# Kernel tuning notes

Measured on AMD Instinct MI355X. Metric: run time of the kernel, lower is better.

The kernel has to match this reference:

```python
import jax, jax.numpy as jnp
import numpy as np

N, E, DIM, HEADS = 50000, 600000, 128, 4
C = DIM // HEADS  # per-head channels = 32
NEG_SLOPE = 0.2
LN_EPS = 1e-5


def setup_inputs() -> dict:
    key = jax.random.key(0)
    ks = jax.random.split(key, 6)
    x = jax.random.normal(ks[0], (N, DIM), dtype=jnp.float32)
    edge_index = jax.random.randint(ks[1], (2, E), 0, N, dtype=jnp.int32)
    W = jax.random.normal(ks[2], (DIM, DIM), dtype=jnp.float32) / np.sqrt(DIM).astype(np.float32)
    b = jnp.zeros((DIM,), jnp.float32)
    att_src = jax.random.normal(ks[3], (HEADS, C), dtype=jnp.float32) * 0.1
    att_dst = jax.random.normal(ks[4], (HEADS, C), dtype=jnp.float32) * 0.1
    gamma = jnp.ones((DIM,), jnp.float32)
    beta = jnp.zeros((DIM,), jnp.float32)
    return {"x": x, "W": W, "b": b, "att_src": att_src, "att_dst": att_dst,
            "gamma": gamma, "beta": beta, "edge_index": edge_index}


def _gat_conv(x, W, b, att_src, att_dst, src, dst):
    # linear projection, per-head view: [N, H, C]
    h = (x @ W).reshape(N, HEADS, C)
    # per-node attention logits: [N, H]
    a_s = jnp.einsum('nhc,hc->nh', h, att_src)
    a_d = jnp.einsum('nhc,hc->nh', h, att_dst)
    # per-edge logits with leaky relu: [Etot, H]
    e = jax.nn.leaky_relu(a_s[src] + a_d[dst], negative_slope=NEG_SLOPE)
    # segment softmax over incoming edges of each dst node
    m = jax.ops.segment_max(e, dst, num_segments=N)
    ez = jnp.exp(e - m[dst])
    denom = jax.ops.segment_sum(ez, dst, num_segments=N) + 1e-16
    alpha = ez / denom[dst]  # [Etot, H]
    # weighted scatter-aggregation: [N, H, C]
    out = jax.ops.segment_sum(alpha[:, :, None] * h[src], dst, num_segments=N)
    return out.reshape(N, DIM) + b


def reference(x, W, b, att_src, att_dst, gamma, beta, edge_index):
    # add self loops (PyG GATConv default add_self_loops=True)
    loops = jnp.arange(N, dtype=edge_index.dtype)
    src = jnp.concatenate([edge_index[0], loops])
    dst = jnp.concatenate([edge_index[1], loops])
    g = _gat_conv(x, W, b, att_src, att_dst, src, dst)
    # residual + GELU (torch exact erf GELU) + LayerNorm; dropout = identity (eval)
    y = x + jax.nn.gelu(g, approximate=False)
    mu = jnp.mean(y, axis=-1, keepdims=True)
    var = jnp.mean(jnp.square(y - mu), axis=-1, keepdims=True)
    return (y - mu) / jnp.sqrt(var + LN_EPS) * gamma + beta
```

## Files before the change

### kernel.cpp

```cpp
#include <hip/hip_runtime.h>
#include <math.h>

#define DIMC 128
#define HEADSC 4

typedef __attribute__((ext_vector_type(8))) short bf16x8;
typedef __attribute__((ext_vector_type(4))) float f32x4;
typedef __attribute__((ext_vector_type(2))) float f32x2;

static __device__ __forceinline__ short f2bf(float f) {
    unsigned u = __builtin_bit_cast(unsigned, f);
    unsigned r = (u + 0x7fff + ((u >> 16) & 1)) >> 16;
    return (short)r;
}
static __device__ __forceinline__ float blo(unsigned q) {
    return __builtin_bit_cast(float, q << 16);
}
static __device__ __forceinline__ float bhi(unsigned q) {
    return __builtin_bit_cast(float, q & 0xffff0000u);
}

__global__ __launch_bounds__(256, 2) void gemm_hist_kernel(
    const float* __restrict__ x, const float* __restrict__ W,
    const float* __restrict__ att_src, const float* __restrict__ att_dst,
    const int* __restrict__ dst, int E,
    unsigned short* __restrict__ hb, float* __restrict__ a_s, float* __restrict__ a_d,
    int* __restrict__ counts, int N, int nstrip)
{
    const int lane = threadIdx.x & 63;
    const int q    = threadIdx.x >> 6;
    const int l15  = lane & 15;
    const int lg   = lane >> 4;

    bf16x8 bfr[2][4];
#pragma unroll
    for (int ct = 0; ct < 2; ++ct) {
#pragma unroll
        for (int kk = 0; kk < 4; ++kk) {
            const float* wp = W + (size_t)(kk * 32 + lg * 8) * DIMC + q * 32 + ct * 16 + l15;
#pragma unroll
            for (int jj = 0; jj < 8; ++jj)
                bfr[ct][kk][jj] = f2bf(wp[(size_t)jj * DIMC]);
        }
    }
    float attS[2], attD[2];
#pragma unroll
    for (int ct = 0; ct < 2; ++ct) {
        attS[ct] = att_src[q * 32 + ct * 16 + l15];
        attD[ct] = att_dst[q * 32 + ct * 16 + l15];
    }

    for (int s = blockIdx.x; s < nstrip; s += gridDim.x) {
        const int row = s * 16 + l15;
        const float* xp = x + (size_t)row * DIMC + lg * 8;
        bf16x8 afr[4];
#pragma unroll
        for (int kk = 0; kk < 4; ++kk) {
            f32x4 v0 = *(const f32x4*)(xp + kk * 32);
            f32x4 v1 = *(const f32x4*)(xp + kk * 32 + 4);
#pragma unroll
            for (int jj = 0; jj < 4; ++jj) {
                afr[kk][jj]     = f2bf(v0[jj]);
                afr[kk][jj + 4] = f2bf(v1[jj]);
            }
        }
        f32x4 acc[2] = {};
#pragma unroll
        for (int ct = 0; ct < 2; ++ct) {
#pragma unroll
            for (int kk = 0; kk < 4; ++kk)
                acc[ct] = __builtin_amdgcn_mfma_f32_16x16x32_bf16(
                    afr[kk], bfr[ct][kk], acc[ct], 0, 0, 0);
        }
        unsigned short* hp = hb + (size_t)(s * 16) * DIMC + q * 32;
#pragma unroll
        for (int ct = 0; ct < 2; ++ct)
#pragma unroll
            for (int reg = 0; reg < 4; ++reg)
                hp[(size_t)(lg * 4 + reg) * DIMC + ct * 16 + l15] =
                    (unsigned short)f2bf(acc[ct][reg]);
#pragma unroll
        for (int reg = 0; reg < 4; ++reg) {
            float sv = fmaf(acc[0][reg], attS[0], acc[1][reg] * attS[1]);
            float dv = fmaf(acc[0][reg], attD[0], acc[1][reg] * attD[1]);
#pragma unroll
            for (int mk = 1; mk < 16; mk <<= 1) {
                sv += __shfl_xor(sv, mk);
                dv += __shfl_xor(dv, mk);
            }
            if (l15 == 0) {
                const int r = s * 16 + lg * 4 + reg;
                a_s[r * HEADSC + q] = sv;
                a_d[r * HEADSC + q] = dv;
            }
        }
    }

    const int tid = blockIdx.x * 256 + threadIdx.x;
    const int stride = gridDim.x * 256;
    if (((E & 3) == 0) && ((((size_t)dst) & 15) == 0)) {
        const int E4 = E >> 2;
        for (int i = tid; i < E4; i += stride) {
            const int4 d4 = ((const int4*)dst)[i];
            atomicAdd(&counts[d4.x], 1);
            atomicAdd(&counts[d4.y], 1);
            atomicAdd(&counts[d4.z], 1);
            atomicAdd(&counts[d4.w], 1);
        }
    } else {
        for (int i = tid; i < E; i += stride) atomicAdd(&counts[dst[i]], 1);
    }
}

__global__ __launch_bounds__(256) void scan1_kernel(
    const int* __restrict__ counts, int* __restrict__ partial, int N)
{
    const int t = threadIdx.x, i = blockIdx.x * 256 + t;
    int v = (i < N) ? counts[i] + 1 : 0;
    int s = v;
#pragma unroll
    for (int mk = 1; mk < 64; mk <<= 1) s += __shfl_xor(s, mk);
    __shared__ int ws[4];
    if ((t & 63) == 0) ws[t >> 6] = s;
    __syncthreads();
    if (t == 0) partial[blockIdx.x] = ws[0] + ws[1] + ws[2] + ws[3];
}

__global__ __launch_bounds__(256) void scan23_kernel(
    const int* __restrict__ counts, const int* __restrict__ partial,
    int* __restrict__ S, int N, int P)
{
    const int t = threadIdx.x;
    const int lane = t & 63, wv = t >> 6;
    __shared__ int ws[4];
    __shared__ int ex[256];

    int pv = (t < P) ? partial[t] : 0;
    int xs = pv;
#pragma unroll
    for (int d = 1; d < 64; d <<= 1) { int tt = __shfl_up(xs, d); if (lane >= d) xs += tt; }
    if (lane == 63) ws[wv] = xs;
    __syncthreads();
    int wof = 0;
#pragma unroll
    for (int w = 0; w < 4; ++w) wof += (w < wv) ? ws[w] : 0;
    ex[t] = wof + xs - pv;
    __syncthreads();
    const int prefix = ex[blockIdx.x];
    __syncthreads();

    const int i = blockIdx.x * 256 + t;
    int v = (i < N) ? counts[i] + 1 : 0;
    int s2 = v;
#pragma unroll
    for (int d = 1; d < 64; d <<= 1) { int tt = __shfl_up(s2, d); if (lane >= d) s2 += tt; }
    if (lane == 63) ws[wv] = s2;
    __syncthreads();
    int wof2 = 0;
#pragma unroll
    for (int w = 0; w < 4; ++w) wof2 += (w < wv) ? ws[w] : 0;
    if (i < N) S[i] = prefix + wof2 + s2 - v;
}

__global__ void scatter_kernel(const int* __restrict__ ei, int E, int N,
                               int* __restrict__ S, int* __restrict__ rec)
{
    const int tid = blockIdx.x * blockDim.x + threadIdx.x;
    const int stride = gridDim.x * blockDim.x;
    if (((E & 3) == 0) && ((((size_t)ei) & 15) == 0)) {
        const int E4 = E >> 2;
        const int4* s4p = (const int4*)ei;
        const int4* d4p = (const int4*)(ei + E);
        for (int i = tid; i < E4; i += stride) {
            const int4 s4 = s4p[i];
            const int4 d4 = d4p[i];
            rec[atomicAdd(&S[d4.x], 1)] = s4.x;
            rec[atomicAdd(&S[d4.y], 1)] = s4.y;
            rec[atomicAdd(&S[d4.z], 1)] = s4.z;
            rec[atomicAdd(&S[d4.w], 1)] = s4.w;
        }
    } else {
        for (int i = tid; i < E; i += stride)
            rec[atomicAdd(&S[ei[E + i]], 1)] = ei[i];
    }
    for (int n = tid; n < N; n += stride)
        rec[atomicAdd(&S[n], 1)] = n;
}

__global__ __launch_bounds__(256) void node_kernel(
    const float* __restrict__ x, const unsigned short* __restrict__ hb,
    const int* __restrict__ S, const int* __restrict__ rec,
    const float* __restrict__ a_s, const float* __restrict__ a_d,
    const float* __restrict__ bias, const float* __restrict__ gamma,
    const float* __restrict__ beta, float* __restrict__ out, int N)
{
    const int wv = threadIdx.x >> 6;
    const int lane = threadIdx.x & 63;
    const int c2 = lane * 2;
    const int head = lane >> 4;

    for (int n = blockIdx.x * 4 + wv; n < N; n += gridDim.x * 4) {
        const int beg = __builtin_amdgcn_readfirstlane(n ? S[n - 1] : 0);
        const int end = __builtin_amdgcn_readfirstlane(S[n]);
        const float adh = a_d[n * HEADSC + head];
        float den = 0.f, A0 = 0.f, A1 = 0.f, B0 = 0.f, B1 = 0.f;
        for (int i = beg; i < end; i += 8) {
            int ss[8];
            float tt[8];
            unsigned qq[8];
#pragma unroll
            for (int u = 0; u < 8; ++u)
                ss[u] = rec[(i + u < end) ? i + u : beg];
#pragma unroll
            for (int u = 0; u < 8; ++u)
                tt[u] = a_s[ss[u] * HEADSC + head] + adh;
#pragma unroll
            for (int u = 0; u < 8; ++u)
                qq[u] = *(const unsigned*)(hb + (size_t)ss[u] * DIMC + c2);
#pragma unroll
            for (int u = 0; u < 8; ++u) {
                float e = tt[u];
                e = (e > 0.f) ? e : 0.2f * e;
                float p = (i + u < end) ? __expf(e) : 0.f;
                den += p;
                if (u & 1) { B0 = fmaf(p, blo(qq[u]), B0); B1 = fmaf(p, bhi(qq[u]), B1); }
                else       { A0 = fmaf(p, blo(qq[u]), A0); A1 = fmaf(p, bhi(qq[u]), A1); }
            }
        }
        const float acc0 = A0 + B0, acc1 = A1 + B1;

        const float inv = 1.f / (den + 1e-16f);
        const f32x2 bi = *(const f32x2*)(bias + c2);
        float g0 = acc0 * inv + bi.x;
        float g1 = acc1 * inv + bi.y;
        const float ge0 = 0.5f * g0 * (1.f + erff(g0 * 0.70710678118654752f));
        const float ge1 = 0.5f * g1 * (1.f + erff(g1 * 0.70710678118654752f));
        const f32x2 xv = *(const f32x2*)(x + (size_t)n * DIMC + c2);
        const float y0 = xv.x + ge0;
        const float y1 = xv.y + ge1;
        float s1 = y0 + y1, s2 = y0 * y0 + y1 * y1;
#pragma unroll
        for (int mk = 1; mk < 64; mk <<= 1) {
            s1 += __shfl_xor(s1, mk);
            s2 += __shfl_xor(s2, mk);
        }
        const float mu = s1 * (1.f / DIMC);
        const float var = s2 * (1.f / DIMC) - mu * mu;
        const float rstd = rsqrtf(var + 1e-5f);
        const f32x2 ga = *(const f32x2*)(gamma + c2);
        const f32x2 be = *(const f32x2*)(beta + c2);
        f32x2 o;
        o.x = (y0 - mu) * rstd * ga.x + be.x;
        o.y = (y1 - mu) * rstd * ga.y + be.y;
        *(f32x2*)(out + (size_t)n * DIMC + c2) = o;
    }
}

extern "C" void kernel_launch(void* const* d_in, const int* in_sizes, int n_in,
                              void* d_out, int out_size, void* d_ws, size_t ws_size,
                              hipStream_t stream)
{
    const float* x       = (const float*)d_in[0];
    const float* W       = (const float*)d_in[1];
    const float* bias    = (const float*)d_in[2];
    const float* att_src = (const float*)d_in[3];
    const float* att_dst = (const float*)d_in[4];
    const float* gamma   = (const float*)d_in[5];
    const float* beta    = (const float*)d_in[6];
    const int*   ei      = (const int*)d_in[7];

    const int N = in_sizes[0] / DIMC;
    const int E = in_sizes[7] / 2;

    unsigned short* hb = (unsigned short*)d_ws;
    float* a_s   = (float*)(hb + (size_t)N * DIMC);
    float* a_d   = a_s + (size_t)N * HEADSC;
    int* counts  = (int*)(a_d + (size_t)N * HEADSC);
    int* S       = counts + N;
    int* partial = S + N;
    int* rec     = partial + 256;

    hipMemsetAsync(counts, 0, sizeof(int) * (size_t)N, stream);

    const int nstrip = (N + 15) / 16;
    gemm_hist_kernel<<<1024, 256, 0, stream>>>(x, W, att_src, att_dst, ei + E, E,
                                               hb, a_s, a_d, counts, N, nstrip);
    const int nb1 = (N + 255) / 256;
    scan1_kernel<<<nb1, 256, 0, stream>>>(counts, partial, N);
    scan23_kernel<<<nb1, 256, 0, stream>>>(counts, partial, S, N, nb1);
    scatter_kernel<<<1024, 256, 0, stream>>>(ei, E, N, S, rec);
    node_kernel<<<(N + 3) / 4, 256, 0, stream>>>(
        x, hb, S, rec, a_s, a_d, bias, gamma, beta, (float*)d_out, N);
}
```

Measured before the change: 202.3 us.

## Coalesce h stores via LDS, split histogram kernel, place self-loops in scan

After: 204.4 us. About the same (+1.0%).

```diff
diff --git a/kernel.cpp b/kernel.cpp
--- a/kernel.cpp
+++ b/kernel.cpp
@@ -20,27 +20,29 @@
     return __builtin_bit_cast(float, q & 0xffff0000u);
 }
 
-__global__ __launch_bounds__(256, 2) void gemm_hist_kernel(
+__global__ __launch_bounds__(256, 2) void gemm_kernel(
     const float* __restrict__ x, const float* __restrict__ W,
     const float* __restrict__ att_src, const float* __restrict__ att_dst,
-    const int* __restrict__ dst, int E,
     unsigned short* __restrict__ hb, float* __restrict__ a_s, float* __restrict__ a_d,
-    int* __restrict__ counts, int N, int nstrip)
-{
+    int nstrip)
+{
+    __shared__ unsigned short wfrag[4][2][4][64][8];
+    __shared__ unsigned short htile[16][128];
+
     const int lane = threadIdx.x & 63;
     const int q    = threadIdx.x >> 6;
     const int l15  = lane & 15;
     const int lg   = lane >> 4;
 
-    bf16x8 bfr[2][4];
 #pragma unroll
     for (int ct = 0; ct < 2; ++ct) {
 #pragma unroll
         for (int kk = 0; kk < 4; ++kk) {
             const float* wp = W + (size_t)(kk * 32 + lg * 8) * DIMC + q * 32 + ct * 16 + l15;
-#pragma unroll
-            for (int jj = 0; jj < 8; ++jj)
-                bfr[ct][kk][jj] = f2bf(wp[(size_t)jj * DIMC]);
+            bf16x8 f;
+#pragma unroll
+            for (int jj = 0; jj < 8; ++jj) f[jj] = f2bf(wp[(size_t)jj * DIMC]);
+            *(bf16x8*)(&wfrag[q][ct][kk][lane][0]) = f;
         }
     }
     float attS[2], attD[2];
@@ -49,6 +51,7 @@
         attS[ct] = att_src[q * 32 + ct * 16 + l15];
         attD[ct] = att_dst[q * 32 + ct * 16 + l15];
     }
+    __syncthreads();
 
     for (int s = blockIdx.x; s < nstrip; s += gridDim.x) {
         const int row = s * 16 + l15;
@@ -68,17 +71,11 @@
 #pragma unroll
         for (int ct = 0; ct < 2; ++ct) {
 #pragma unroll
-            for (int kk = 0; kk < 4; ++kk)
-                acc[ct] = __builtin_amdgcn_mfma_f32_16x16x32_bf16(
-                    afr[kk], bfr[ct][kk], acc[ct], 0, 0, 0);
-        }
-        unsigned short* hp = hb + (size_t)(s * 16) * DIMC + q * 32;
-#pragma unroll
-        for (int ct = 0; ct < 2; ++ct)
-#pragma unroll
-            for (int reg = 0; reg < 4; ++reg)
-                hp[(size_t)(lg * 4 + reg) * DIMC + ct * 16 + l15] =
-                    (unsigned short)f2bf(acc[ct][reg]);
+            for (int kk = 0; kk < 4; ++kk) {
+                bf16x8 b = *(const bf16x8*)(&wfrag[q][ct][kk][lane][0]);
+                acc[ct] = __builtin_amdgcn_mfma_f32_16x16x32_bf16(afr[kk], b, acc[ct], 0, 0, 0);
+            }
+        }
 #pragma unroll
         for (int reg = 0; reg < 4; ++reg) {
             float sv = fmaf(acc[0][reg], attS[0], acc[1][reg] * attS[1]);
@@ -94,10 +91,25 @@
                 a_d[r * HEADSC + q] = dv;
             }
         }
-    }
-
-    const int tid = blockIdx.x * 256 + threadIdx.x;
-    const int stride = gridDim.x * 256;
+        __syncthreads();
+#pragma unroll
+        for (int ct = 0; ct < 2; ++ct)
+#pragma unroll
+            for (int reg = 0; reg < 4; ++reg)
+                htile[lg * 4 + reg][q * 32 + ct * 16 + l15] =
+                    (unsigned short)f2bf(acc[ct][reg]);
+        __syncthreads();
+        const int r2  = threadIdx.x >> 4;
+        const int c2b = (threadIdx.x & 15) * 8;
+        bf16x8 v = *(const bf16x8*)(&htile[r2][c2b]);
+        *(bf16x8*)(hb + (size_t)(s * 16 + r2) * DIMC + c2b) = v;
+    }
+}
+
+__global__ void hist_kernel(const int* __restrict__ dst, int E, int* __restrict__ counts)
+{
+    const int tid = blockIdx.x * blockDim.x + threadIdx.x;
+    const int stride = gridDim.x * blockDim.x;
     if (((E & 3) == 0) && ((((size_t)dst) & 15) == 0)) {
         const int E4 = E >> 2;
         for (int i = tid; i < E4; i += stride) {
@@ -128,7 +140,7 @@
 
 __global__ __launch_bounds__(256) void scan23_kernel(
     const int* __restrict__ counts, const int* __restrict__ partial,
-    int* __restrict__ S, int N, int P)
+    int* __restrict__ S, int* __restrict__ rec, int N, int P)
 {
     const int t = threadIdx.x;
     const int lane = t & 63, wv = t >> 6;
@@ -159,10 +171,14 @@
     int wof2 = 0;
 #pragma unroll
     for (int w = 0; w < 4; ++w) wof2 += (w < wv) ? ws[w] : 0;
-    if (i < N) S[i] = prefix + wof2 + s2 - v;
-}
-
-__global__ void scatter_kernel(const int* __restrict__ ei, int E, int N,
+    if (i < N) {
+        const int base = prefix + wof2 + s2 - v;
+        rec[base] = i;
+        S[i] = base + 1;
+    }
+}
+
+__global__ void scatter_kernel(const int* __restrict__ ei, int E,
                                int* __restrict__ S, int* __restrict__ rec)
 {
     const int tid = blockIdx.x * blockDim.x + threadIdx.x;
@@ -183,8 +199,6 @@
         for (int i = tid; i < E; i += stride)
             rec[atomicAdd(&S[ei[E + i]], 1)] = ei[i];
     }
-    for (int n = tid; n < N; n += stride)
-        rec[atomicAdd(&S[n], 1)] = n;
 }
 
 __global__ __launch_bounds__(256) void node_kernel(
@@ -283,12 +297,12 @@
     hipMemsetAsync(counts, 0, sizeof(int) * (size_t)N, stream);
 
     const int nstrip = (N + 15) / 16;
-    gemm_hist_kernel<<<1024, 256, 0, stream>>>(x, W, att_src, att_dst, ei + E, E,
-                                               hb, a_s, a_d, counts, N, nstrip);
+    gemm_kernel<<<1024, 256, 0, stream>>>(x, W, att_src, att_dst, hb, a_s, a_d, nstrip);
+    hist_kernel<<<1024, 256, 0, stream>>>(ei + E, E, counts);
     const int nb1 = (N + 255) / 256;
     scan1_kernel<<<nb1, 256, 0, stream>>>(counts, partial, N);
-    scan23_kernel<<<nb1, 256, 0, stream>>>(counts, partial, S, N, nb1);
-    scatter_kernel<<<1024, 256, 0, stream>>>(ei, E, N, S, rec);
+    scan23_kernel<<<nb1, 256, 0, stream>>>(counts, partial, S, rec, N, nb1);
+    scatter_kernel<<<1024, 256, 0, stream>>>(ei, E, S, rec);
     node_kernel<<<(N + 3) / 4, 256, 0, stream>>>(
         x, hb, S, rec, a_s, a_d, bias, gamma, beta, (float*)d_out, N);
 }
```
